# Kernel optimization log

Hardware: AMD Instinct MI355X
Metric: run time of the kernel (lower is better)

The kernel has to match this reference:

```python
import jax, jax.numpy as jnp
import numpy as np

B, H, W, DIM = 16, 28, 28, 256
HEADS, K = 8, 7
HD = DIM // HEADS
MLP = int(DIM * 4.0)
EPS = 1e-5


def setup_inputs() -> dict:
    key = jax.random.key(0)
    ks = jax.random.split(key, 8)
    s = 0.02
    return {
        "x": jax.random.normal(ks[0], (B, H, W, DIM), jnp.float32),
        "norm1_w": jnp.ones((DIM,), jnp.float32),
        "norm1_b": jnp.zeros((DIM,), jnp.float32),
        "qkv_w": jax.random.normal(ks[1], (3 * DIM, DIM), jnp.float32) * s,
        "qkv_b": jnp.zeros((3 * DIM,), jnp.float32),
        "rpb": jax.random.normal(ks[2], (HEADS, 2 * K - 1, 2 * K - 1), jnp.float32) * s,
        "proj_w": jax.random.normal(ks[3], (DIM, DIM), jnp.float32) * s,
        "proj_b": jnp.zeros((DIM,), jnp.float32),
        "norm2_w": jnp.ones((DIM,), jnp.float32),
        "norm2_b": jnp.zeros((DIM,), jnp.float32),
        "fc1_w": jax.random.normal(ks[4], (MLP, DIM), jnp.float32) * s,
        "fc1_b": jnp.zeros((MLP,), jnp.float32),
        "fc2_w": jax.random.normal(ks[5], (DIM, MLP), jnp.float32) * s,
        "fc2_b": jnp.zeros((DIM,), jnp.float32),
    }


def _ln(x, w, b):
    m = jnp.mean(x, axis=-1, keepdims=True)
    v = jnp.var(x, axis=-1, keepdims=True)  # biased, as torch LayerNorm
    return (x - m) * jax.lax.rsqrt(v + EPS) * w + b


def _window_idx(n):
    # NATTEN border handling: window shifts so every query has exactly K neighbors
    start = jnp.clip(jnp.arange(n) - K // 2, 0, n - K)  # [n]
    idx = start[:, None] + jnp.arange(K)                # [n, K] absolute neighbor index
    rel = idx - jnp.arange(n)[:, None] + (K - 1)        # [n, K] rpb index in [0, 2K-2]
    return idx, rel


def _neighborhood_attn(x, qkv_w, qkv_b, rpb, proj_w, proj_b):
    b, h, w, c = x.shape
    qkv = (x @ qkv_w.T + qkv_b).reshape(b, h, w, 3, HEADS, HD)
    q, k, v = qkv[:, :, :, 0], qkv[:, :, :, 1], qkv[:, :, :, 2]  # [b,h,w,heads,hd]
    q = q * (HD ** -0.5)
    idx_h, rel_h = _window_idx(h)
    idx_w, rel_w = _window_idx(w)
    # gather K/V neighborhoods: [b,h,K,w,K,heads,hd]
    kwin = k[:, idx_h][:, :, :, idx_w]
    vwin = v[:, idx_h][:, :, :, idx_w]
    # logits per query (i,j) over its KxK window
    attn = jnp.einsum('bijhd,biajchd->bhijac', q, kwin)  # [b,heads,h,w,K,K]
    bias = rpb[:, rel_h]                 # [heads,h,K,2K-1]
    bias = bias[:, :, :, rel_w]          # [heads,h,K,w,K]
    bias = bias.transpose(0, 1, 3, 2, 4) # [heads,h,w,K,K]
    attn = attn + bias[None]
    attn = jax.nn.softmax(attn.reshape(b, HEADS, h, w, K * K), axis=-1)
    attn = attn.reshape(b, HEADS, h, w, K, K)
    out = jnp.einsum('bhijac,biajchd->bijhd', attn, vwin).reshape(b, h, w, c)
    return out @ proj_w.T + proj_b


def reference(x, norm1_w, norm1_b, qkv_w, qkv_b, rpb, proj_w, proj_b,
              norm2_w, norm2_b, fc1_w, fc1_b, fc2_w, fc2_b):
    shortcut = x
    x = _ln(x, norm1_w, norm1_b)
    x = shortcut + _neighborhood_attn(x, qkv_w, qkv_b, rpb, proj_w, proj_b)
    h = _ln(x, norm2_w, norm2_b) @ fc1_w.T + fc1_b
    h = jax.nn.gelu(h, approximate=False)  # torch nn.GELU default (erf)
    return x + (h @ fc2_w.T + fc2_b)
```

## Files before the change

### kernel.cpp

```cpp
#include <hip/hip_runtime.h>
#include <hip/hip_bf16.h>
#include <math.h>

#define DIM   256
#define HEADS 8
#define HD    32
#define KW    7
#define HH    28
#define WW    28
#define BBATCH 16
#define NTOK  (BBATCH*HH*WW)
#define MLPD  1024
#define EPSLN 1e-5f
#define QSCALE 0.17677669529663687f

#define AS1 __attribute__((address_space(1)))
#define AS3 __attribute__((address_space(3)))

typedef __attribute__((ext_vector_type(8))) short short8;
typedef __attribute__((ext_vector_type(4))) float f32x4;

__device__ __forceinline__ float b2f(unsigned short u) {
  union { float f; unsigned u; } x; x.u = ((unsigned)u) << 16; return x.f;
}
__device__ __forceinline__ unsigned short f2b(float f) {
  union { float f; unsigned u; } x; x.f = f;
  unsigned lsb = (x.u >> 16) & 1;
  x.u += 0x7fffu + lsb;
  return (unsigned short)(x.u >> 16);
}
__device__ __forceinline__ bool probe_f32(const unsigned short* p) { return p[0] == 0; }

__device__ __forceinline__ void gll16(const unsigned short* g, unsigned short* l) {
  __builtin_amdgcn_global_load_lds((const AS1 unsigned*)(const void*)g,
                                   (AS3 unsigned*)(void*)l, 16, 0, 0);
}

__global__ __launch_bounds__(256) void pre_kernel(const void* s0, const void* s1,
                                                  const void* s2, const void* s3,
                                                  unsigned short* d0, unsigned short* d1,
                                                  unsigned short* d2, unsigned short* d3,
                                                  const void* p0, const void* p1, const void* p2,
                                                  const void* p3, const void* p4, const void* p5,
                                                  const void* p6, const void* p7, const void* p8,
                                                  float* __restrict__ pack,
                                                  const void* __restrict__ x,
                                                  unsigned short* __restrict__ xn1,
                                                  float* __restrict__ bias_t,
                                                  const unsigned short* __restrict__ probe)
{
  const bool isf32 = probe_f32(probe);
  const int blk = blockIdx.x;
  const int t = threadIdx.x;
  if (blk < 768) {
    const int gi = (blk * 256 + t) * 4;
    const void* src; unsigned short* dst; int loc;
    if (gi < 196608)      { src = s0; dst = d0; loc = gi; }
    else if (gi < 262144) { src = s1; dst = d1; loc = gi - 196608; }
    else if (gi < 524288) { src = s2; dst = d2; loc = gi - 262144; }
    else                  { src = s3; dst = d3; loc = gi - 524288; }
    if (isf32) {
      float4 v = *(const float4*)((const float*)src + loc);
      ushort4 o; o.x = f2b(v.x); o.y = f2b(v.y); o.z = f2b(v.z); o.w = f2b(v.w);
      *(ushort4*)(dst + loc) = o;
    } else {
      *(ushort4*)(dst + loc) = *(const ushort4*)((const unsigned short*)src + loc);
    }
  } else if (blk < 777) {
    const int seg = blk - 768;
    const void* srcs[9] = {p0, p1, p2, p3, p4, p5, p6, p7, p8};
    const int offs[9] = {0, 256, 512, 1280, 1536, 1792, 2048, 3072, 3328};
    const int lens[9] = {256, 256, 768, 256, 256, 256, 1024, 256, 1352};
    const void* s = srcs[seg];
    const int off = offs[seg], len = lens[seg];
    for (int i = t; i < len; i += 256)
      pack[off + i] = isf32 ? ((const float*)s)[i] : b2f(((const unsigned short*)s)[i]);
  } else if (blk < 3913) {
    const int wave = t >> 6, lane = t & 63;
    const int tok = (blk - 777) * 4 + wave;
    const int c0 = lane * 4;
    float v[4];
    if (isf32) {
      const float4 f = *(const float4*)((const float*)x + (size_t)tok * DIM + c0);
      v[0] = f.x; v[1] = f.y; v[2] = f.z; v[3] = f.w;
    } else {
      ushort4 u = *(const ushort4*)((const unsigned short*)x + (size_t)tok * DIM + c0);
      v[0] = b2f(u.x); v[1] = b2f(u.y); v[2] = b2f(u.z); v[3] = b2f(u.w);
    }
    float s  = v[0] + v[1] + v[2] + v[3];
    float s2 = v[0]*v[0] + v[1]*v[1] + v[2]*v[2] + v[3]*v[3];
    #pragma unroll
    for (int m = 32; m; m >>= 1) { s += __shfl_xor(s, m); s2 += __shfl_xor(s2, m); }
    const float mean = s * (1.0f / DIM);
    const float var  = s2 * (1.0f / DIM) - mean * mean;
    const float rstd = rsqrtf(var + EPSLN);
    float wv[4], bv[4];
    if (isf32) {
      const float4 a = *(const float4*)((const float*)p0 + c0);
      const float4 c = *(const float4*)((const float*)p1 + c0);
      wv[0]=a.x; wv[1]=a.y; wv[2]=a.z; wv[3]=a.w;
      bv[0]=c.x; bv[1]=c.y; bv[2]=c.z; bv[3]=c.w;
    } else {
      ushort4 a = *(const ushort4*)((const unsigned short*)p0 + c0);
      ushort4 c = *(const ushort4*)((const unsigned short*)p1 + c0);
      wv[0]=b2f(a.x); wv[1]=b2f(a.y); wv[2]=b2f(a.z); wv[3]=b2f(a.w);
      bv[0]=b2f(c.x); bv[1]=b2f(c.y); bv[2]=b2f(c.z); bv[3]=b2f(c.w);
    }
    ushort4 o;
    o.x = f2b((v[0] - mean) * rstd * wv[0] + bv[0]);
    o.y = f2b((v[1] - mean) * rstd * wv[1] + bv[1]);
    o.z = f2b((v[2] - mean) * rstd * wv[2] + bv[2]);
    o.w = f2b((v[3] - mean) * rstd * wv[3] + bv[3]);
    *(ushort4*)(xn1 + (size_t)tok * DIM + c0) = o;
  } else {
    const int ph = blk - 3913;
    const int p  = ph >> 3, h = ph & 7;
    const int i0 = 2 * p;
    const int si0 = min(max(i0 - 3, 0), 21);
    float* bt = bias_t + (size_t)ph * (224 * 64);
    for (int e = 0; e < 56; ++e) {
      const int idx = e * 256 + t;
      const int kv = idx >> 6;
      const int q  = idx & 63;
      const int isub = q >> 5;
      const int cq = q & 31;
      const int iq = i0 + isub;
      const int siq = min(max(iq - 3, 0), 21);
      const int sj  = min(max(cq - 3, 0), 21);
      const int rr  = (kv * 2341) >> 16;
      const int ar  = si0 + rr;
      const int ck  = kv - rr * 28;
      const int dr = ar - siq, dc = ck - sj;
      const bool valid = (cq < 28) && (dr >= 0) && (dr < 7) && (dc >= 0) && (dc < 7);
      float val = -1e30f;
      if (valid) {
        const int ridx = h * 169 + (ar - iq + 6) * 13 + (ck - cq + 6);
        val = isf32 ? ((const float*)p8)[ridx] : b2f(((const unsigned short*)p8)[ridx]);
      }
      bt[idx] = val;
    }
  }
}

__global__ __launch_bounds__(256) void ln_kernel(const float* __restrict__ in,
                                                 const float* __restrict__ w,
                                                 const float* __restrict__ b,
                                                 unsigned short* __restrict__ out)
{
  const int t = threadIdx.x;
  const int wave = t >> 6, lane = t & 63;
  const int tok = blockIdx.x * 4 + wave;
  const int c0 = lane * 4;
  const float4 f = *(const float4*)(in + (size_t)tok * DIM + c0);
  float v[4] = {f.x, f.y, f.z, f.w};
  float s  = v[0] + v[1] + v[2] + v[3];
  float s2 = v[0]*v[0] + v[1]*v[1] + v[2]*v[2] + v[3]*v[3];
  #pragma unroll
  for (int m = 32; m; m >>= 1) { s += __shfl_xor(s, m); s2 += __shfl_xor(s2, m); }
  const float mean = s * (1.0f / DIM);
  const float var  = s2 * (1.0f / DIM) - mean * mean;
  const float rstd = rsqrtf(var + EPSLN);
  const float4 wv = *(const float4*)(w + c0);
  const float4 bv = *(const float4*)(b + c0);
  ushort4 o;
  o.x = f2b((v[0] - mean) * rstd * wv.x + bv.x);
  o.y = f2b((v[1] - mean) * rstd * wv.y + bv.y);
  o.z = f2b((v[2] - mean) * rstd * wv.z + bv.z);
  o.w = f2b((v[3] - mean) * rstd * wv.w + bv.w);
  *(ushort4*)(out + (size_t)tok * DIM + c0) = o;
}

template<int MODE>
__global__ __launch_bounds__(256) void gemm_kernel(const unsigned short* __restrict__ A,
                                                   const unsigned short* __restrict__ W,
                                                   const float* __restrict__ bias,
                                                   const void* __restrict__ resid,
                                                   void* __restrict__ out,
                                                   int N, int K,
                                                   const unsigned short* __restrict__ probe)
{
  __shared__ unsigned short As[2][128 * 32];
  __shared__ unsigned short Bs[2][64 * 32];
  const int t = threadIdx.x;
  const int wave = t >> 6, lane = t & 63;
  const int wm = wave >> 1, wn = wave & 1;
  const int m0 = blockIdx.x * 128;
  const int n0 = blockIdx.y * 64;
  const int lm = lane & 15;
  const int kb = (lane >> 4) * 8;

  const int srow = t >> 2;
  const int scol = (t & 3) * 8;
  const unsigned short* Ag0 = A + (size_t)(m0 + srow) * K + scol;
  const unsigned short* Ag1 = A + (size_t)(m0 + 64 + srow) * K + scol;
  const unsigned short* Bg  = W + (size_t)(n0 + srow) * K + scol;

  const int NS = K >> 5;
  gll16(Ag0, &As[0][t * 8]);
  gll16(Ag1, &As[0][2048 + t * 8]);
  gll16(Bg,  &Bs[0][t * 8]);

  f32x4 acc[4][2] = {};
  int cur = 0;
  for (int s = 0; s < NS; ++s) {
    __syncthreads();
    if (s + 1 < NS) {
      const int kk = (s + 1) << 5;
      gll16(Ag0 + kk, &As[cur ^ 1][t * 8]);
      gll16(Ag1 + kk, &As[cur ^ 1][2048 + t * 8]);
      gll16(Bg + kk,  &Bs[cur ^ 1][t * 8]);
    }
    short8 a[4], b[2];
    #pragma unroll
    for (int mf = 0; mf < 4; ++mf)
      a[mf] = *(const short8*)(const void*)&As[cur][(wm * 64 + mf * 16 + lm) * 32 + kb];
    #pragma unroll
    for (int nf = 0; nf < 2; ++nf)
      b[nf] = *(const short8*)(const void*)&Bs[cur][(wn * 32 + nf * 16 + lm) * 32 + kb];
    #pragma unroll
    for (int mf = 0; mf < 4; ++mf) {
      #pragma unroll
      for (int nf = 0; nf < 2; ++nf)
        acc[mf][nf] = __builtin_amdgcn_mfma_f32_16x16x32_bf16(a[mf], b[nf], acc[mf][nf], 0, 0, 0);
    }
    cur ^= 1;
  }

  const bool isf32 = (MODE == 1 || MODE == 3) ? probe_f32(probe) : false;
  const int col = lane & 15;
  const int rb  = (lane >> 4) * 4;
  #pragma unroll
  for (int mf = 0; mf < 4; ++mf) {
    #pragma unroll
    for (int nf = 0; nf < 2; ++nf) {
      const int n = n0 + wn * 32 + nf * 16 + col;
      const float bv = bias[n];
      #pragma unroll
      for (int j = 0; j < 4; ++j) {
        const int m = m0 + wm * 64 + mf * 16 + rb + j;
        const size_t off = (size_t)m * N + n;
        float v = acc[mf][nf][j] + bv;
        if (MODE == 0) {
          ((unsigned short*)out)[off] = f2b(n < 256 ? v * QSCALE : v);
        } else if (MODE == 1) {
          v += isf32 ? ((const float*)resid)[off] : b2f(((const unsigned short*)resid)[off]);
          ((float*)out)[off] = v;
        } else if (MODE == 2) {
          v = 0.5f * v * (1.0f + erff(v * 0.70710678118654752f));
          ((unsigned short*)out)[off] = f2b(v);
        } else {
          v += ((const float*)resid)[off];
          if (isf32) ((float*)out)[off] = v;
          else       ((unsigned short*)out)[off] = f2b(v);
        }
      }
    }
  }
}

__global__ __launch_bounds__(256) void attn_kernel(const unsigned short* __restrict__ qkv,
                                                   const float* __restrict__ bias_t,
                                                   unsigned short* __restrict__ out)
{
  __shared__ unsigned short K_lds[896 * 8];
  __shared__ unsigned short Vt_lds[32 * 232];
  __shared__ unsigned short P_lds[64 * 232];

  const int raw = blockIdx.x;
  const int bid = (raw & 7) * 224 + (raw >> 3);
  const int b  = bid & 15;
  const int ph = bid >> 4;
  const int p  = ph >> 3;
  const int h  = ph & 7;
  const int i0 = 2 * p;
  const int t = threadIdx.x;
  const int wave = t >> 6, lane = t & 63;
  const int lm = lane & 15, g = lane >> 4;
  const int kb = g * 8;
  const int si0 = min(max(i0 - 3, 0), 21);
  const int si1 = min(max(i0 - 2, 0), 21);
  const int nch = (si1 + 7 - si0) * 112;

  const unsigned short* kg = qkv + ((size_t)(b * 784 + si0 * 28)) * 768 + 256 + h * 32;
  const unsigned short* vg = kg + 256;

  const int c0 = t, c1 = 256 + t, c2 = 512 + t, c3 = 768 + t;
  const bool has3 = c3 < nch;
  uint4 v0 = *(const uint4*)(const void*)(vg + (size_t)(c0 >> 2) * 768 + (c0 & 3) * 8);
  uint4 v1 = *(const uint4*)(const void*)(vg + (size_t)(c1 >> 2) * 768 + (c1 & 3) * 8);
  uint4 v2 = *(const uint4*)(const void*)(vg + (size_t)(c2 >> 2) * 768 + (c2 & 3) * 8);
  uint4 v3;
  if (has3) v3 = *(const uint4*)(const void*)(vg + (size_t)(c3 >> 2) * 768 + (c3 & 3) * 8);

  {
    int gk;
    gk = c0 ^ ((c0 >> 3) & 7); gll16(kg + (size_t)(gk >> 2) * 768 + (gk & 3) * 8, &K_lds[c0 * 8]);
    gk = c1 ^ ((c1 >> 3) & 7); gll16(kg + (size_t)(gk >> 2) * 768 + (gk & 3) * 8, &K_lds[c1 * 8]);
    gk = c2 ^ ((c2 >> 3) & 7); gll16(kg + (size_t)(gk >> 2) * 768 + (gk & 3) * 8, &K_lds[c2 * 8]);
    if (has3) { gk = c3 ^ ((c3 >> 3) & 7); gll16(kg + (size_t)(gk >> 2) * 768 + (gk & 3) * 8, &K_lds[c3 * 8]); }
  }

  if (nch == 784) {
    if (t < 112) *(uint4*)(void*)&K_lds[(784 + t) * 8] = make_uint4(0, 0, 0, 0);
    const int ch = t >> 3, of = 196 + (t & 7) * 4;
    *(uint2*)(void*)&Vt_lds[ch * 232 + of] = make_uint2(0, 0);
  }

  {
    const unsigned uu0[4] = {v0.x, v0.y, v0.z, v0.w};
    const unsigned uu1[4] = {v1.x, v1.y, v1.z, v1.w};
    const unsigned uu2[4] = {v2.x, v2.y, v2.z, v2.w};
    #pragma unroll
    for (int e = 0; e < 4; ++e) {
      Vt_lds[((c0 & 3) * 8 + 2*e)     * 232 + (c0 >> 2)] = (unsigned short)(uu0[e] & 0xffffu);
      Vt_lds[((c0 & 3) * 8 + 2*e + 1) * 232 + (c0 >> 2)] = (unsigned short)(uu0[e] >> 16);
      Vt_lds[((c1 & 3) * 8 + 2*e)     * 232 + (c1 >> 2)] = (unsigned short)(uu1[e] & 0xffffu);
      Vt_lds[((c1 & 3) * 8 + 2*e + 1) * 232 + (c1 >> 2)] = (unsigned short)(uu1[e] >> 16);
      Vt_lds[((c2 & 3) * 8 + 2*e)     * 232 + (c2 >> 2)] = (unsigned short)(uu2[e] & 0xffffu);
      Vt_lds[((c2 & 3) * 8 + 2*e + 1) * 232 + (c2 >> 2)] = (unsigned short)(uu2[e] >> 16);
    }
    if (has3) {
      const unsigned uu3[4] = {v3.x, v3.y, v3.z, v3.w};
      #pragma unroll
      for (int e = 0; e < 4; ++e) {
        Vt_lds[((c3 & 3) * 8 + 2*e)     * 232 + (c3 >> 2)] = (unsigned short)(uu3[e] & 0xffffu);
        Vt_lds[((c3 & 3) * 8 + 2*e + 1) * 232 + (c3 >> 2)] = (unsigned short)(uu3[e] >> 16);
      }
    }
  }

  const int qcol_l = min((wave & 1) * 16 + lm, 27);
  const int iq = i0 + (wave >> 1);
  const short8 qa = *(const short8*)(const void*)(qkv + ((size_t)(b * 784 + iq * 28 + qcol_l)) * 768 + h * 32 + kb);

  __syncthreads();

  f32x4 s[14];
  #pragma unroll
  for (int n = 0; n < 14; ++n) {
    const int sl0 = (n * 16 + lm) * 4 + g;
    const int sl = sl0 ^ ((sl0 >> 3) & 7);
    const short8 kf = *(const short8*)(const void*)&K_lds[sl * 8];
    f32x4 z = {0.f, 0.f, 0.f, 0.f};
    s[n] = __builtin_amdgcn_mfma_f32_16x16x32_bf16(qa, kf, z, 0, 0, 0);
  }

  const float* bt = bias_t + (size_t)ph * (224 * 64);
  const int qb = wave * 16 + g * 4;
  float mx[4] = {-1e30f, -1e30f, -1e30f, -1e30f};
  #pragma unroll
  for (int n = 0; n < 14; ++n) {
    const f32x4 bb = *(const f32x4*)(const void*)&bt[(n * 16 + lm) * 64 + qb];
    #pragma unroll
    for (int jj = 0; jj < 4; ++jj) {
      const float r = s[n][jj] + bb[jj];
      s[n][jj] = r;
      mx[jj] = fmaxf(mx[jj], r);
    }
  }
  float sm[4];
  #pragma unroll
  for (int jj = 0; jj < 4; ++jj) {
    float m = mx[jj];
    m = fmaxf(m, __shfl_xor(m, 1)); m = fmaxf(m, __shfl_xor(m, 2));
    m = fmaxf(m, __shfl_xor(m, 4)); m = fmaxf(m, __shfl_xor(m, 8));
    float acc = 0.f;
    #pragma unroll
    for (int n = 0; n < 14; ++n) {
      const float e = __expf(s[n][jj] - m);
      acc += e;
      P_lds[(qb + jj) * 232 + n * 16 + lm] = f2b(e);
    }
    acc += __shfl_xor(acc, 1); acc += __shfl_xor(acc, 2);
    acc += __shfl_xor(acc, 4); acc += __shfl_xor(acc, 8);
    sm[jj] = acc;
  }

  #pragma unroll
  for (int nto = 0; nto < 2; ++nto) {
    f32x4 o = {0.f, 0.f, 0.f, 0.f};
    #pragma unroll
    for (int ks = 0; ks < 7; ++ks) {
      const short8 pa = *(const short8*)(const void*)&P_lds[(wave * 16 + lm) * 232 + ks * 32 + kb];
      const short8 vb = *(const short8*)(const void*)&Vt_lds[(nto * 16 + lm) * 232 + ks * 32 + kb];
      o = __builtin_amdgcn_mfma_f32_16x16x32_bf16(pa, vb, o, 0, 0, 0);
    }
    #pragma unroll
    for (int jj = 0; jj < 4; ++jj) {
      const int qc = (wave & 1) * 16 + g * 4 + jj;
      if (qc < 28) {
        const float inv = 1.0f / sm[jj];
        out[((size_t)(b * 784 + iq * 28 + qc)) * 256 + h * 32 + nto * 16 + lm] = f2b(o[jj] * inv);
      }
    }
  }
}

extern "C" void kernel_launch(void* const* d_in, const int* in_sizes, int n_in,
                              void* d_out, int out_size, void* d_ws, size_t ws_size,
                              hipStream_t stream)
{
  const unsigned short* probe = (const unsigned short*)d_in[1];

  char* ws = (char*)d_ws;
  unsigned short* wqkv_c = (unsigned short*)(ws);
  unsigned short* wproj_c= (unsigned short*)(ws + 393216);
  unsigned short* wfc1_c = (unsigned short*)(ws + 524288);
  unsigned short* wfc2_c = (unsigned short*)(ws + 1048576);
  float*          pack   = (float*)         (ws + 1572864);
  float*          bias_t = (float*)         (ws + 1593344);
  unsigned short* xn1    = (unsigned short*)(ws + 8015872);
  unsigned short* qkv    = (unsigned short*)(ws + 14438400);
  float*          out1   = (float*)         (ws + 33705984);
  unsigned short* hbuf   = (unsigned short*)(ws + 46551040);
  unsigned short* att    = xn1;
  unsigned short* xn2    = qkv;

  const float* p_qkvb = pack + 512;
  const float* p_projb= pack + 1280;
  const float* p_n2w  = pack + 1536;
  const float* p_n2b  = pack + 1792;
  const float* p_fc1b = pack + 2048;
  const float* p_fc2b = pack + 3072;

  pre_kernel<<<4025, 256, 0, stream>>>(d_in[3], d_in[6], d_in[10], d_in[12],
                                       wqkv_c, wproj_c, wfc1_c, wfc2_c,
                                       d_in[1], d_in[2], d_in[4], d_in[7], d_in[8], d_in[9],
                                       d_in[11], d_in[13], d_in[5], pack,
                                       d_in[0], xn1, bias_t, probe);
  gemm_kernel<0><<<dim3(NTOK / 128, 768 / 64), 256, 0, stream>>>(xn1, wqkv_c, p_qkvb, nullptr, qkv, 768, 256, probe);
  attn_kernel<<<BBATCH * (HH / 2) * HEADS, 256, 0, stream>>>(qkv, bias_t, att);
  gemm_kernel<1><<<dim3(NTOK / 128, DIM / 64), 256, 0, stream>>>(att, wproj_c, p_projb, d_in[0], out1, DIM, 256, probe);
  ln_kernel<<<NTOK / 4, 256, 0, stream>>>(out1, p_n2w, p_n2b, xn2);
  gemm_kernel<2><<<dim3(NTOK / 128, MLPD / 64), 256, 0, stream>>>(xn2, wfc1_c, p_fc1b, nullptr, hbuf, MLPD, 256, probe);
  gemm_kernel<3><<<dim3(NTOK / 128, DIM / 64), 256, 0, stream>>>(hbuf, wfc2_c, p_fc2b, out1, d_out, DIM, MLPD, probe);
}
```

Baseline: 138.3 us.

## Add XOR-swizzled LDS layout and 128-wide N tiles for QKV and FC1 GEMMs

Adds an XOR swizzle to how global-to-LDS loads are placed in shared memory, with matching swizzled fragment reads, to reduce LDS bank conflicts on the MFMA operand loads. Templates the GEMM on tile width BN and uses 128-wide N tiles for the wide QKV and FC1 GEMMs, so each block reuses its A tile across twice as many output columns. The larger tile doubles the B shared-memory buffer and accumulator registers and halves the grid for those GEMMs, which may lower occupancy.

```diff
diff --git a/kernel.cpp b/kernel.cpp
--- a/kernel.cpp
+++ b/kernel.cpp
@@ -170,7 +170,7 @@
   *(ushort4*)(out + (size_t)tok * DIM + c0) = o;
 }
 
-template<int MODE>
+template<int BN, int MODE>
 __global__ __launch_bounds__(256) void gemm_kernel(const unsigned short* __restrict__ A,
                                                    const unsigned short* __restrict__ W,
                                                    const float* __restrict__ bias,
@@ -179,28 +179,33 @@
                                                    int N, int K,
                                                    const unsigned short* __restrict__ probe)
 {
+  constexpr int NF = BN / 32;
   __shared__ unsigned short As[2][128 * 32];
-  __shared__ unsigned short Bs[2][64 * 32];
+  __shared__ unsigned short Bs[2][BN * 32];
   const int t = threadIdx.x;
   const int wave = t >> 6, lane = t & 63;
   const int wm = wave >> 1, wn = wave & 1;
   const int m0 = blockIdx.x * 128;
-  const int n0 = blockIdx.y * 64;
+  const int n0 = blockIdx.y * BN;
   const int lm = lane & 15;
-  const int kb = (lane >> 4) * 8;
-
-  const int srow = t >> 2;
-  const int scol = (t & 3) * 8;
+  const int g  = lane >> 4;
+  const int kb = g * 8;
+
+  const int gc = t ^ ((t >> 3) & 7);
+  const int srow = gc >> 2;
+  const int scol = (gc & 3) * 8;
   const unsigned short* Ag0 = A + (size_t)(m0 + srow) * K + scol;
   const unsigned short* Ag1 = A + (size_t)(m0 + 64 + srow) * K + scol;
-  const unsigned short* Bg  = W + (size_t)(n0 + srow) * K + scol;
+  const unsigned short* Bg0 = W + (size_t)(n0 + srow) * K + scol;
+  const unsigned short* Bg1 = W + (size_t)(n0 + (BN == 128 ? 64 : 0) + srow) * K + scol;
 
   const int NS = K >> 5;
   gll16(Ag0, &As[0][t * 8]);
   gll16(Ag1, &As[0][2048 + t * 8]);
-  gll16(Bg,  &Bs[0][t * 8]);
-
-  f32x4 acc[4][2] = {};
+  gll16(Bg0, &Bs[0][t * 8]);
+  if (BN == 128) gll16(Bg1, &Bs[0][2048 + t * 8]);
+
+  f32x4 acc[4][NF] = {};
   int cur = 0;
   for (int s = 0; s < NS; ++s) {
     __syncthreads();
@@ -208,19 +213,28 @@
       const int kk = (s + 1) << 5;
       gll16(Ag0 + kk, &As[cur ^ 1][t * 8]);
       gll16(Ag1 + kk, &As[cur ^ 1][2048 + t * 8]);
-      gll16(Bg + kk,  &Bs[cur ^ 1][t * 8]);
-    }
-    short8 a[4], b[2];
-    #pragma unroll
-    for (int mf = 0; mf < 4; ++mf)
-      a[mf] = *(const short8*)(const void*)&As[cur][(wm * 64 + mf * 16 + lm) * 32 + kb];
-    #pragma unroll
-    for (int nf = 0; nf < 2; ++nf)
-      b[nf] = *(const short8*)(const void*)&Bs[cur][(wn * 32 + nf * 16 + lm) * 32 + kb];
+      gll16(Bg0 + kk, &Bs[cur ^ 1][t * 8]);
+      if (BN == 128) gll16(Bg1 + kk, &Bs[cur ^ 1][2048 + t * 8]);
+    }
+    short8 a[4], b[NF];
+    #pragma unroll
+    for (int mf = 0; mf < 4; ++mf) {
+      const int row = wm * 64 + mf * 16 + lm;
+      const int c = (row & 63) * 4 + g;
+      const int sl = c ^ ((c >> 3) & 7);
+      a[mf] = *(const short8*)(const void*)&As[cur][(row >> 6) * 2048 + sl * 8];
+    }
+    #pragma unroll
+    for (int nf = 0; nf < NF; ++nf) {
+      const int row = wn * (BN / 2) + nf * 16 + lm;
+      const int c = (row & 63) * 4 + g;
+      const int sl = c ^ ((c >> 3) & 7);
+      b[nf] = *(const short8*)(const void*)&Bs[cur][(row >> 6) * 2048 + sl * 8];
+    }
     #pragma unroll
     for (int mf = 0; mf < 4; ++mf) {
       #pragma unroll
-      for (int nf = 0; nf < 2; ++nf)
+      for (int nf = 0; nf < NF; ++nf)
         acc[mf][nf] = __builtin_amdgcn_mfma_f32_16x16x32_bf16(a[mf], b[nf], acc[mf][nf], 0, 0, 0);
     }
     cur ^= 1;
@@ -232,8 +246,8 @@
   #pragma unroll
   for (int mf = 0; mf < 4; ++mf) {
     #pragma unroll
-    for (int nf = 0; nf < 2; ++nf) {
-      const int n = n0 + wn * 32 + nf * 16 + col;
+    for (int nf = 0; nf < NF; ++nf) {
+      const int n = n0 + wn * (BN / 2) + nf * 16 + col;
       const float bv = bias[n];
       #pragma unroll
       for (int j = 0; j < 4; ++j) {
@@ -428,10 +442,10 @@
                                        d_in[1], d_in[2], d_in[4], d_in[7], d_in[8], d_in[9],
                                        d_in[11], d_in[13], d_in[5], pack,
                                        d_in[0], xn1, bias_t, probe);
-  gemm_kernel<0><<<dim3(NTOK / 128, 768 / 64), 256, 0, stream>>>(xn1, wqkv_c, p_qkvb, nullptr, qkv, 768, 256, probe);
+  gemm_kernel<128, 0><<<dim3(NTOK / 128, 768 / 128), 256, 0, stream>>>(xn1, wqkv_c, p_qkvb, nullptr, qkv, 768, 256, probe);
   attn_kernel<<<BBATCH * (HH / 2) * HEADS, 256, 0, stream>>>(qkv, bias_t, att);
-  gemm_kernel<1><<<dim3(NTOK / 128, DIM / 64), 256, 0, stream>>>(att, wproj_c, p_projb, d_in[0], out1, DIM, 256, probe);
+  gemm_kernel<64, 1><<<dim3(NTOK / 128, DIM / 64), 256, 0, stream>>>(att, wproj_c, p_projb, d_in[0], out1, DIM, 256, probe);
   ln_kernel<<<NTOK / 4, 256, 0, stream>>>(out1, p_n2w, p_n2b, xn2);
-  gemm_kernel<2><<<dim3(NTOK / 128, MLPD / 64), 256, 0, stream>>>(xn2, wfc1_c, p_fc1b, nullptr, hbuf, MLPD, 256, probe);
-  gemm_kernel<3><<<dim3(NTOK / 128, DIM / 64), 256, 0, stream>>>(hbuf, wfc2_c, p_fc2b, out1, d_out, DIM, MLPD, probe);
-}
+  gemm_kernel<128, 2><<<dim3(NTOK / 128, MLPD / 128), 256, 0, stream>>>(xn2, wfc1_c, p_fc1b, nullptr, hbuf, MLPD, 256, probe);
+  gemm_kernel<64, 3><<<dim3(NTOK / 128, DIM / 64), 256, 0, stream>>>(hbuf, wfc2_c, p_fc2b, out1, d_out, DIM, MLPD, probe);
+}
```

Result: no change. 139.5 us (+0.8%).
